# Performance work log

Hardware: AMD Instinct MI355X
Metric: run time of the kernel (lower is better)

## Reference

```python
import jax, jax.numpy as jnp
import numpy as np

B, S, D = 4, 2048, 2048
E = 8
H = (4 * D) // E  # per-expert hidden = 1024
DS = D // 2       # shared-layer hidden
LOAD_BALANCE_WEIGHT = 0.01


def setup_inputs() -> dict:
    key = jax.random.key(0)
    ks = jax.random.split(key, 12)
    s = 0.02
    return {
        "x": jax.random.normal(ks[0], (B, S, D), dtype=jnp.float32),
        "W_router": jax.random.normal(ks[1], (D, E), dtype=jnp.float32) * s,
        "b_router": jnp.zeros((E,), dtype=jnp.float32),
        "W1": jax.random.normal(ks[2], (E, D, H), dtype=jnp.float32) * s,
        "b1": jnp.zeros((E, H), dtype=jnp.float32),
        "W2": jax.random.normal(ks[3], (E, H, D), dtype=jnp.float32) * s,
        "b2": jnp.zeros((E, D), dtype=jnp.float32),
        "Ws1": jax.random.normal(ks[4], (D, DS), dtype=jnp.float32) * s,
        "bs1": jnp.zeros((DS,), dtype=jnp.float32),
        "Ws2": jax.random.normal(ks[5], (DS, D), dtype=jnp.float32) * s,
        "bs2": jnp.zeros((D,), dtype=jnp.float32),
    }


def reference(x, W_router, b_router, W1, b1, W2, b2, Ws1, bs1, Ws2, bs2):
    # Router: soft weights over all experts (soft-MoE, every expert runs).
    router_logits = jnp.einsum("bsd,de->bse", x, W_router) + b_router
    router_weights = jax.nn.softmax(router_logits, axis=-1)  # (B,S,E)

    # Shared branch: Linear -> GELU (exact, matching torch default) -> Linear.
    shared = jax.nn.gelu(jnp.einsum("bsd,dh->bsh", x, Ws1) + bs1, approximate=False)
    shared = jnp.einsum("bsh,hd->bsd", shared, Ws2) + bs2

    # All experts as one batched GEMM pair (fuses the torch Python loop).
    h = jax.nn.gelu(jnp.einsum("bsd,edh->bseh", x, W1) + b1, approximate=False)  # (B,S,E,H)
    expert_out = jnp.einsum("bseh,ehd->bsed", h, W2) + b2  # (B,S,E,D)

    # Softmax-weighted combine + scaled shared residual (dropout=0 / eval).
    weighted = jnp.einsum("bsed,bse->bsd", expert_out, router_weights)
    output = weighted + 0.1 * shared

    # Load-balance aux loss: MSE between mean usage and uniform.
    expert_usage = router_weights.mean(axis=(0, 1))  # (E,)
    uniform = jnp.full_like(expert_usage, 1.0 / E)
    aux_loss = jnp.mean((expert_usage - uniform) ** 2) * LOAD_BALANCE_WEIGHT
    return output, aux_loss
```

## Files before the change

kernel.cpp:

```cpp
#include <hip/hip_runtime.h>
#include <hip/hip_bf16.h>
#include <stdint.h>

#define DEV static __device__ __forceinline__

typedef __attribute__((ext_vector_type(4))) float f32x4;
typedef __attribute__((ext_vector_type(8))) short bf16x8;
typedef __attribute__((ext_vector_type(4))) float float4v;

constexpr int NBATCH = 4;
constexpr int SEQ    = 2048;
constexpr int DIM    = 2048;
constexpr int NEXP   = 8;
constexpr int HEXP   = 1024;
constexpr int DSH    = 1024;
constexpr int NTOK   = NBATCH * SEQ;
constexpr int JEXP   = NEXP * HEXP;
constexpr int JTOT   = JEXP + DSH;

DEV short f2bf(float f) {
  __hip_bfloat16 b = __float2bfloat16(f);
  union { __hip_bfloat16 b; short s; } u; u.b = b; return u.s;
}

DEV void gload16(const void* gp, const void* lp) {
  __builtin_amdgcn_global_load_lds(
      (__attribute__((address_space(1))) void*)(uintptr_t)gp,
      (__attribute__((address_space(3))) void*)(uint32_t)(uintptr_t)lp,
      16, 0, 0);
}

__global__ void conv_x_k(const float* __restrict__ x, short* __restrict__ xb) {
  size_t i = (size_t)blockIdx.x * blockDim.x + threadIdx.x;
  const float4v* s = reinterpret_cast<const float4v*>(x) + i * 2;
  float4v a = s[0], b = s[1];
  bf16x8 o;
  o[0] = f2bf(a.x); o[1] = f2bf(a.y); o[2] = f2bf(a.z); o[3] = f2bf(a.w);
  o[4] = f2bf(b.x); o[5] = f2bf(b.y); o[6] = f2bf(b.z); o[7] = f2bf(b.w);
  *reinterpret_cast<bf16x8*>(xb + i * 8) = o;
}

__global__ __launch_bounds__(256) void router_k(
    const float* __restrict__ x, const float* __restrict__ Wr,
    const float* __restrict__ br, float* __restrict__ rw,
    float* __restrict__ auxs) {
  const int wave = threadIdx.x >> 6, lane = threadIdx.x & 63;
  const int t = blockIdx.x * 4 + wave;
  const float* xr = x + (size_t)t * DIM;
  float a[NEXP];
#pragma unroll
  for (int e = 0; e < NEXP; ++e) a[e] = 0.f;
  for (int i = 0; i < DIM / 64; ++i) {
    int k = i * 64 + lane;
    float xv = xr[k];
    const float* w = Wr + (size_t)k * NEXP;
#pragma unroll
    for (int e = 0; e < NEXP; ++e) a[e] = fmaf(xv, w[e], a[e]);
  }
#pragma unroll
  for (int e = 0; e < NEXP; ++e) {
    float v = a[e];
#pragma unroll
    for (int off = 32; off > 0; off >>= 1) v += __shfl_xor(v, off, 64);
    a[e] = v + br[e];
  }
  float mx = a[0];
#pragma unroll
  for (int e = 1; e < NEXP; ++e) mx = fmaxf(mx, a[e]);
  float s = 0.f;
#pragma unroll
  for (int e = 0; e < NEXP; ++e) { a[e] = expf(a[e] - mx); s += a[e]; }
  float inv = 1.f / s;
#pragma unroll
  for (int e = 0; e < NEXP; ++e) a[e] *= inv;
  if (lane == 0) {
#pragma unroll
    for (int e = 0; e < NEXP; ++e) rw[(size_t)t * NEXP + e] = a[e];
  }
  __shared__ float blk[NEXP];
  if (threadIdx.x < NEXP) blk[threadIdx.x] = 0.f;
  __syncthreads();
  if (lane == 0) {
#pragma unroll
    for (int e = 0; e < NEXP; ++e) atomicAdd(&blk[e], a[e]);
  }
  __syncthreads();
  if (threadIdx.x < NEXP) atomicAdd(&auxs[threadIdx.x], blk[threadIdx.x]);
}

__global__ void zero_aux_k(float* auxs) {
  if (threadIdx.x < NEXP) auxs[threadIdx.x] = 0.f;
}

__global__ void fin_aux_k(const float* __restrict__ auxs, float* __restrict__ dst) {
  if (threadIdx.x == 0) {
    float s = 0.f;
    for (int e = 0; e < NEXP; ++e) {
      float u = auxs[e] / (float)NTOK - (1.0f / NEXP);
      s += u * u;
    }
    dst[0] = (s / NEXP) * 0.01f;
  }
}

__global__ __launch_bounds__(256) void conv_w1_k(
    const float* __restrict__ W1, const float* __restrict__ Ws1,
    short* __restrict__ dst, int jbase, int jc) {
  __shared__ float tile[64][65];
  const int j0 = jbase + blockIdx.x * 64;
  const int k0 = blockIdx.y * 64;
  const int tx = threadIdx.x & 63;
  const int ty = threadIdx.x >> 6;
#pragma unroll
  for (int i = 0; i < 16; ++i) {
    int kk = ty * 16 + i;
    int j = j0 + tx, k = k0 + kk;
    float v;
    if (j < JEXP) {
      int e = j >> 10, h = j & 1023;
      v = W1[(size_t)e * DIM * HEXP + (size_t)k * HEXP + h];
    } else {
      v = Ws1[(size_t)k * DSH + (j - JEXP)];
    }
    tile[kk][tx] = v;
  }
  __syncthreads();
#pragma unroll
  for (int i = 0; i < 16; ++i) {
    int jj = ty * 16 + i;
    int jloc = j0 - jbase + jj;
    dst[(size_t)jloc * DIM + k0 + tx] = f2bf(tile[tx][jj]);
  }
}

__global__ __launch_bounds__(256) void conv_w2_k(
    const float* __restrict__ W2, const float* __restrict__ Ws2,
    short* __restrict__ dst, int jbase, int jc) {
  __shared__ float tile[64][65];
  const int j0 = jbase + blockIdx.x * 64;
  const int d0 = blockIdx.y * 64;
  const int tx = threadIdx.x & 63;
  const int ty = threadIdx.x >> 6;
#pragma unroll
  for (int i = 0; i < 16; ++i) {
    int jj = ty * 16 + i;
    int j = j0 + jj;
    float v;
    if (j < JEXP) {
      int e = j >> 10, h = j & 1023;
      v = W2[(size_t)e * HEXP * DIM + (size_t)h * DIM + d0 + tx];
    } else {
      v = 0.1f * Ws2[(size_t)(j - JEXP) * DIM + d0 + tx];
    }
    tile[jj][tx] = v;
  }
  __syncthreads();
#pragma unroll
  for (int i = 0; i < 16; ++i) {
    int dd = ty * 16 + i;
    dst[(size_t)(d0 + dd) * jc + (j0 - jbase) + tx] = f2bf(tile[tx][dd]);
  }
}

template <int MODE>
__global__ __launch_bounds__(512, 4) void gemmA(
    const short* __restrict__ A, const short* __restrict__ Bt, int K,
    const float* __restrict__ rw,
    const float* __restrict__ bias_a, const float* __restrict__ bias_b,
    short* __restrict__ hOut, int jbase, int jc,
    float* __restrict__ out, int nx) {
  extern __shared__ short smem[];
  const int tid = threadIdx.x;
  const int w = tid >> 6, lane = tid & 63;
  const int wm = w >> 1, wn = w & 1;

  const int nwg = nx * (NTOK / 256);
  int orig = blockIdx.x;
  const int q = nwg >> 3, r = nwg & 7;
  const int xcd = orig & 7, off = orig >> 3;
  const int bid = (xcd < r ? xcd * (q + 1) : r * (q + 1) + (xcd - r) * q) + off;
  const int bx = bid % nx, by = bid / nx;
  const int m0 = by * 256, n0 = bx * 128;

  f32x4 acc[4][4] = {};

  const int aoff = ((lane & 15) << 6) + ((((lane >> 4) ^ ((lane >> 1) & 3)) & 3) << 4);

  const int srow = lane >> 2;
  const int scol = (((lane & 3) ^ ((lane >> 3) & 3)) << 3);
  const short* gA0 = A + (size_t)(m0 + w * 32 + srow) * K + scol;
  const short* gB0 = Bt + (size_t)(n0 + w * 16 + srow) * K + scol;
  const size_t k16 = (size_t)16 * K;
  const int NT = K >> 5;

#define STG(TT) { const int sl_ = (TT) & 1; const size_t co_ = (size_t)(TT) << 5;  \
    short* lA_ = smem + sl_ * 12288 + w * 1024;                                    \
    short* lB_ = smem + sl_ * 12288 + 8192 + w * 512;                              \
    gload16(gA0 + co_, lA_);                                                       \
    gload16(gA0 + k16 + co_, lA_ + 512);                                           \
    gload16(gB0 + co_, lB_); }

  STG(0);

  for (int t = 0; t < NT; ++t) {
    asm volatile("s_waitcnt vmcnt(0)" ::: "memory");
    __builtin_amdgcn_s_barrier();
    asm volatile("" ::: "memory");
    if (t + 1 < NT) STG(t + 1);
    const char* base = (const char*)(smem + (t & 1) * 12288);
    const char* pa = base + wm * 4096 + aoff;
    const char* pb = base + 16384 + wn * 4096 + aoff;
    bf16x8 bf[4], af[4];
#pragma unroll
    for (int n = 0; n < 4; ++n) bf[n] = *(const bf16x8*)(pb + n * 1024);
#pragma unroll
    for (int m = 0; m < 4; ++m) af[m] = *(const bf16x8*)(pa + m * 1024);
#pragma unroll
    for (int m = 0; m < 4; ++m)
#pragma unroll
      for (int n = 0; n < 4; ++n)
        acc[m][n] = __builtin_amdgcn_mfma_f32_16x16x32_bf16(af[m], bf[n], acc[m][n], 0, 0, 0);
  }
#undef STG

  const int r0 = (lane >> 4) * 4;
  const int ccol = lane & 15;
#pragma unroll
  for (int m = 0; m < 4; ++m) {
#pragma unroll
    for (int i = 0; i < 4; ++i) {
      const int trow = m0 + wm * 64 + m * 16 + r0 + i;
      if (MODE == 0) {
#pragma unroll
        for (int n = 0; n < 4; ++n) {
          const int col = n0 + wn * 64 + n * 16 + ccol;
          const int j = jbase + col;
          float v = acc[m][n][i];
          float bias = (j < JEXP) ? bias_a[j] : bias_b[j - JEXP];
          float val = v + bias;
          float g = 0.5f * val * (1.0f + erff(val * 0.70710678118654752f));
          float wgt = (j < JEXP) ? rw[(size_t)trow * NEXP + (j >> 10)] : 1.0f;
          hOut[(size_t)trow * jc + col] = f2bf(g * wgt);
        }
      } else if (MODE == 1) {
        float rw8[8];
#pragma unroll
        for (int e = 0; e < 8; ++e) rw8[e] = rw[(size_t)trow * NEXP + e];
#pragma unroll
        for (int n = 0; n < 4; ++n) {
          const int col = n0 + wn * 64 + n * 16 + ccol;
          float bias = 0.1f * bias_b[col];
#pragma unroll
          for (int e = 0; e < 8; ++e) bias += rw8[e] * bias_a[(size_t)e * DIM + col];
          out[(size_t)trow * DIM + col] = acc[m][n][i] + bias;
        }
      } else {
#pragma unroll
        for (int n = 0; n < 4; ++n) {
          const int col = n0 + wn * 64 + n * 16 + ccol;
          out[(size_t)trow * DIM + col] += acc[m][n][i];
        }
      }
    }
  }
}

template <int MODE>
__global__ __launch_bounds__(256) void gemm128(
    const short* __restrict__ A, const short* __restrict__ Bt, int K,
    const float* __restrict__ rw,
    const float* __restrict__ bias_a, const float* __restrict__ bias_b,
    short* __restrict__ hOut, int jbase, int jc,
    float* __restrict__ out) {
  __shared__ short As[128 * 64];
  __shared__ short Bs[128 * 64];
  const int tid = threadIdx.x;
  const int wave = tid >> 6, lane = tid & 63;
  const int wr = wave >> 1, wc = wave & 1;
  const int m0 = blockIdx.y * 128;
  const int n0 = blockIdx.x * 128;

  f32x4 acc[4][4] = {};

  const int srow = wave * 8 + (lane >> 3);
  const int scol = (((lane & 7) ^ (lane >> 3)) << 3);
  const short* gA = A + (size_t)(m0 + srow) * K + scol;
  const short* gB = Bt + (size_t)(n0 + srow) * K + scol;
  const short* lA = As + wave * 512;
  const short* lB = Bs + wave * 512;

  const int rrow = lane & 15;
  const int koff = lane >> 4;
  const int kxor = lane & 7;

  for (int kt = 0; kt < K; kt += 64) {
#pragma unroll
    for (int i = 0; i < 4; ++i) {
      gload16(gA + (size_t)i * 32 * K + kt, lA + i * 2048);
      gload16(gB + (size_t)i * 32 * K + kt, lB + i * 2048);
    }
    asm volatile("s_waitcnt vmcnt(0)" ::: "memory");
    __syncthreads();
#pragma unroll
    for (int kk = 0; kk < 2; ++kk) {
      bf16x8 af[4], bfv[4];
#pragma unroll
      for (int m = 0; m < 4; ++m) {
        int row = wr * 64 + m * 16 + rrow;
        int chunk = (kk * 4 + koff) ^ kxor;
        af[m] = *reinterpret_cast<const bf16x8*>(&As[row * 64 + chunk * 8]);
      }
#pragma unroll
      for (int n = 0; n < 4; ++n) {
        int row = wc * 64 + n * 16 + rrow;
        int chunk = (kk * 4 + koff) ^ kxor;
        bfv[n] = *reinterpret_cast<const bf16x8*>(&Bs[row * 64 + chunk * 8]);
      }
#pragma unroll
      for (int m = 0; m < 4; ++m)
#pragma unroll
        for (int n = 0; n < 4; ++n)
          acc[m][n] = __builtin_amdgcn_mfma_f32_16x16x32_bf16(af[m], bfv[n], acc[m][n], 0, 0, 0);
    }
    __syncthreads();
  }

  const int r0 = (lane >> 4) * 4;
  const int ccol = lane & 15;
#pragma unroll
  for (int m = 0; m < 4; ++m) {
#pragma unroll
    for (int n = 0; n < 4; ++n) {
      int col = n0 + wc * 64 + n * 16 + ccol;
#pragma unroll
      for (int i = 0; i < 4; ++i) {
        int t = m0 + wr * 64 + m * 16 + r0 + i;
        float v = acc[m][n][i];
        if (MODE == 0) {
          int j = jbase + col;
          float bias = (j < JEXP) ? bias_a[j] : bias_b[j - JEXP];
          float val = v + bias;
          float g = 0.5f * val * (1.0f + erff(val * 0.70710678118654752f));
          float wg = (j < JEXP) ? rw[(size_t)t * NEXP + (j >> 10)] : 1.0f;
          hOut[(size_t)t * jc + col] = f2bf(g * wg);
        } else if (MODE == 1) {
          float bias = 0.1f * bias_b[col];
#pragma unroll
          for (int e = 0; e < NEXP; ++e)
            bias += rw[(size_t)t * NEXP + e] * bias_a[(size_t)e * DIM + col];
          out[(size_t)t * DIM + col] = v + bias;
        } else {
          out[(size_t)t * DIM + col] += v;
        }
      }
    }
  }
}

extern "C" void kernel_launch(void* const* d_in, const int* in_sizes, int n_in,
                              void* d_out, int out_size, void* d_ws, size_t ws_size,
                              hipStream_t stream) {
  const float* x   = (const float*)d_in[0];
  const float* Wr  = (const float*)d_in[1];
  const float* br  = (const float*)d_in[2];
  const float* W1  = (const float*)d_in[3];
  const float* b1  = (const float*)d_in[4];
  const float* W2  = (const float*)d_in[5];
  const float* b2  = (const float*)d_in[6];
  const float* Ws1 = (const float*)d_in[7];
  const float* bs1 = (const float*)d_in[8];
  const float* Ws2 = (const float*)d_in[9];
  const float* bs2 = (const float*)d_in[10];
  float* out = (float*)d_out;

  char* wsb = (char*)d_ws;
  short* xb   = (short*)wsb;
  float* rw   = (float*)(wsb + 33554432);
  float* auxs = (float*)(wsb + 33816576);
  const size_t need_fixed = 33816832ull;

  const int jcands[8] = {9216, 4608, 3072, 2304, 1536, 768, 512, 256};
  int jc = 256;
  for (int ci = 0; ci < 8; ++ci) {
    if (need_fixed + (size_t)jcands[ci] * 24576ull <= ws_size) { jc = jcands[ci]; break; }
  }
  const int nc = JTOT / jc;
  short* w1t  = (short*)(wsb + need_fixed);
  short* w2t  = w1t + (size_t)jc * DIM;
  short* hbuf = w2t + (size_t)DIM * jc;

  bool big = true;
  {
    auto* f0 = gemmA<0>; auto* f1 = gemmA<1>; auto* f2 = gemmA<2>;
    if (hipFuncSetAttribute(reinterpret_cast<const void*>(f0),
                            hipFuncAttributeMaxDynamicSharedMemorySize, 49152) != hipSuccess) big = false;
    if (hipFuncSetAttribute(reinterpret_cast<const void*>(f1),
                            hipFuncAttributeMaxDynamicSharedMemorySize, 49152) != hipSuccess) big = false;
    if (hipFuncSetAttribute(reinterpret_cast<const void*>(f2),
                            hipFuncAttributeMaxDynamicSharedMemorySize, 49152) != hipSuccess) big = false;
  }

  zero_aux_k<<<1, 64, 0, stream>>>(auxs);
  conv_x_k<<<(NTOK * DIM / 8) / 256, 256, 0, stream>>>(x, xb);
  router_k<<<NTOK / 4, 256, 0, stream>>>(x, Wr, br, rw, auxs);
  fin_aux_k<<<1, 64, 0, stream>>>(auxs, out + (size_t)NTOK * DIM);

  for (int c = 0; c < nc; ++c) {
    const int jbase = c * jc;
    conv_w1_k<<<dim3(jc / 64, DIM / 64), 256, 0, stream>>>(W1, Ws1, w1t, jbase, jc);
    conv_w2_k<<<dim3(jc / 64, DIM / 64), 256, 0, stream>>>(W2, Ws2, w2t, jbase, jc);
    if (big) {
      const int nx1 = jc / 128, ny = NTOK / 256;
      gemmA<0><<<nx1 * ny, 512, 49152, stream>>>(
          xb, w1t, DIM, rw, b1, bs1, hbuf, jbase, jc, nullptr, nx1);
      const int nx2 = DIM / 128;
      if (c == 0) {
        gemmA<1><<<nx2 * ny, 512, 49152, stream>>>(
            hbuf, w2t, jc, rw, b2, bs2, nullptr, 0, jc, out, nx2);
      } else {
        gemmA<2><<<nx2 * ny, 512, 49152, stream>>>(
            hbuf, w2t, jc, rw, nullptr, nullptr, nullptr, 0, jc, out, nx2);
      }
    } else {
      gemm128<0><<<dim3(jc / 128, NTOK / 128), 256, 0, stream>>>(
          xb, w1t, DIM, rw, b1, bs1, hbuf, jbase, jc, nullptr);
      if (c == 0) {
        gemm128<1><<<dim3(DIM / 128, NTOK / 128), 256, 0, stream>>>(
            hbuf, w2t, jc, rw, b2, bs2, nullptr, 0, jc, out);
      } else {
        gemm128<2><<<dim3(DIM / 128, NTOK / 128), 256, 0, stream>>>(
            hbuf, w2t, jc, rw, nullptr, nullptr, nullptr, 0, jc, out);
      }
    }
  }
}
```

Measured before the change: 802.9 us.

## Use 4 waves with 128x64 warp tiles and triple-buffered LDS in gemmA

Halves the workgroup to 256 threads, so each wave now computes a 128x64 output tile (8x4 MFMA accumulators) instead of 64x64. The LDS pipeline goes from double to triple buffering, with a partial vmcnt wait so global loads for two tiles ahead stay in flight. Dynamic LDS grows to 72KB and the launch bounds change to (256,2). The aim is more reuse of each fragment and better hiding of load latency, at the cost of higher VGPR pressure and fewer waves per CU.

New measurement: 963.7 us. 20.0% more time.

```diff
diff --git a/kernel.cpp b/kernel.cpp
--- a/kernel.cpp
+++ b/kernel.cpp
@@ -163,7 +163,7 @@
 }
 
 template <int MODE>
-__global__ __launch_bounds__(512, 4) void gemmA(
+__global__ __launch_bounds__(256, 2) void gemmA(
     const short* __restrict__ A, const short* __restrict__ Bt, int K,
     const float* __restrict__ rw,
     const float* __restrict__ bias_a, const float* __restrict__ bias_b,
@@ -182,54 +182,67 @@
   const int bx = bid % nx, by = bid / nx;
   const int m0 = by * 256, n0 = bx * 128;
 
-  f32x4 acc[4][4] = {};
+  f32x4 acc[8][4] = {};
 
   const int aoff = ((lane & 15) << 6) + ((((lane >> 4) ^ ((lane >> 1) & 3)) & 3) << 4);
 
   const int srow = lane >> 2;
   const int scol = (((lane & 3) ^ ((lane >> 3) & 3)) << 3);
-  const short* gA0 = A + (size_t)(m0 + w * 32 + srow) * K + scol;
-  const short* gB0 = Bt + (size_t)(n0 + w * 16 + srow) * K + scol;
+  const short* gA0 = A + (size_t)(m0 + w * 64 + srow) * K + scol;
+  const short* gB0 = Bt + (size_t)(n0 + w * 32 + srow) * K + scol;
   const size_t k16 = (size_t)16 * K;
   const int NT = K >> 5;
 
-#define STG(TT) { const int sl_ = (TT) & 1; const size_t co_ = (size_t)(TT) << 5;  \
-    short* lA_ = smem + sl_ * 12288 + w * 1024;                                    \
-    short* lB_ = smem + sl_ * 12288 + 8192 + w * 512;                              \
-    gload16(gA0 + co_, lA_);                                                       \
-    gload16(gA0 + k16 + co_, lA_ + 512);                                           \
-    gload16(gB0 + co_, lB_); }
-
-  STG(0);
+#define STG(GOFF, SOFF) {                                                          \
+    short* lA_ = smem + (SOFF) + w * 2048;                                         \
+    short* lB_ = smem + (SOFF) + 8192 + w * 1024;                                  \
+    gload16(gA0 + (GOFF), lA_);                                                    \
+    gload16(gA0 + k16 + (GOFF), lA_ + 512);                                        \
+    gload16(gA0 + 2 * k16 + (GOFF), lA_ + 1024);                                   \
+    gload16(gA0 + 3 * k16 + (GOFF), lA_ + 1536);                                   \
+    gload16(gB0 + (GOFF), lB_);                                                    \
+    gload16(gB0 + k16 + (GOFF), lB_ + 512); }
+
+  STG(0, 0);
+  if (NT > 1) STG(32, 12288);
+
+  int curOff = 0;
+  int stgOff = 24576;
+  size_t gOff = 64;
 
   for (int t = 0; t < NT; ++t) {
-    asm volatile("s_waitcnt vmcnt(0)" ::: "memory");
+    if (t < NT - 1) { asm volatile("s_waitcnt vmcnt(6)" ::: "memory"); }
+    else            { asm volatile("s_waitcnt vmcnt(0)" ::: "memory"); }
     __builtin_amdgcn_s_barrier();
     asm volatile("" ::: "memory");
-    if (t + 1 < NT) STG(t + 1);
-    const char* base = (const char*)(smem + (t & 1) * 12288);
-    const char* pa = base + wm * 4096 + aoff;
+    if (t + 2 < NT) STG(gOff, stgOff);
+    const char* base = (const char*)(smem + curOff);
+    const char* pa = base + wm * 8192 + aoff;
     const char* pb = base + 16384 + wn * 4096 + aoff;
-    bf16x8 bf[4], af[4];
+    bf16x8 bf[4], af[8];
 #pragma unroll
     for (int n = 0; n < 4; ++n) bf[n] = *(const bf16x8*)(pb + n * 1024);
 #pragma unroll
-    for (int m = 0; m < 4; ++m) af[m] = *(const bf16x8*)(pa + m * 1024);
-#pragma unroll
-    for (int m = 0; m < 4; ++m)
+    for (int m = 0; m < 8; ++m) af[m] = *(const bf16x8*)(pa + m * 1024);
+#pragma unroll
+    for (int m = 0; m < 8; ++m)
 #pragma unroll
       for (int n = 0; n < 4; ++n)
         acc[m][n] = __builtin_amdgcn_mfma_f32_16x16x32_bf16(af[m], bf[n], acc[m][n], 0, 0, 0);
+    int nxt = curOff;
+    curOff = (curOff == 24576) ? 0 : curOff + 12288;
+    stgOff = nxt;
+    gOff += 32;
   }
 #undef STG
 
   const int r0 = (lane >> 4) * 4;
   const int ccol = lane & 15;
 #pragma unroll
-  for (int m = 0; m < 4; ++m) {
+  for (int m = 0; m < 8; ++m) {
 #pragma unroll
     for (int i = 0; i < 4; ++i) {
-      const int trow = m0 + wm * 64 + m * 16 + r0 + i;
+      const int trow = m0 + wm * 128 + m * 16 + r0 + i;
       if (MODE == 0) {
 #pragma unroll
         for (int n = 0; n < 4; ++n) {
@@ -393,11 +406,11 @@
   {
     auto* f0 = gemmA<0>; auto* f1 = gemmA<1>; auto* f2 = gemmA<2>;
     if (hipFuncSetAttribute(reinterpret_cast<const void*>(f0),
-                            hipFuncAttributeMaxDynamicSharedMemorySize, 49152) != hipSuccess) big = false;
+                            hipFuncAttributeMaxDynamicSharedMemorySize, 73728) != hipSuccess) big = false;
     if (hipFuncSetAttribute(reinterpret_cast<const void*>(f1),
-                            hipFuncAttributeMaxDynamicSharedMemorySize, 49152) != hipSuccess) big = false;
+                            hipFuncAttributeMaxDynamicSharedMemorySize, 73728) != hipSuccess) big = false;
     if (hipFuncSetAttribute(reinterpret_cast<const void*>(f2),
-                            hipFuncAttributeMaxDynamicSharedMemorySize, 49152) != hipSuccess) big = false;
+                            hipFuncAttributeMaxDynamicSharedMemorySize, 73728) != hipSuccess) big = false;
   }
 
   zero_aux_k<<<1, 64, 0, stream>>>(auxs);
@@ -411,14 +424,14 @@
     conv_w2_k<<<dim3(jc / 64, DIM / 64), 256, 0, stream>>>(W2, Ws2, w2t, jbase, jc);
     if (big) {
       const int nx1 = jc / 128, ny = NTOK / 256;
-      gemmA<0><<<nx1 * ny, 512, 49152, stream>>>(
+      gemmA<0><<<nx1 * ny, 256, 73728, stream>>>(
           xb, w1t, DIM, rw, b1, bs1, hbuf, jbase, jc, nullptr, nx1);
       const int nx2 = DIM / 128;
       if (c == 0) {
-        gemmA<1><<<nx2 * ny, 512, 49152, stream>>>(
+        gemmA<1><<<nx2 * ny, 256, 73728, stream>>>(
             hbuf, w2t, jc, rw, b2, bs2, nullptr, 0, jc, out, nx2);
       } else {
-        gemmA<2><<<nx2 * ny, 512, 49152, stream>>>(
+        gemmA<2><<<nx2 * ny, 256, 73728, stream>>>(
             hbuf, w2t, jc, rw, nullptr, nullptr, nullptr, 0, jc, out, nx2);
       }
     } else {
```
